# Performance work log

Hardware: AMD Instinct MI355X
Metric: run time of the kernel (lower is better)

## Reference

```python
import math
import jax, jax.numpy as jnp
import numpy as np

CH_IN = 32
CH_OUT = 32
K = 3
P = 4
STRIDE = 2
ITER = 3
FINAL_LAMBDA = 0.01
EPS = 1e-8
LOG_2PI = math.log(2.0 * math.pi)


def _conv_stat(x):
    # Conv2d(ch_in, ch_in, K, stride, bias=False) with constant weight 1/K^2, VALID padding
    w = jnp.full((CH_IN, CH_IN, K, K), 1.0 / (K * K), dtype=x.dtype)
    return jax.lax.conv_general_dilated(
        x, w, window_strides=(STRIDE, STRIDE), padding='VALID',
        dimension_numbers=('NCHW', 'OIHW', 'NCHW'))


def setup_inputs() -> dict:
    key = jax.random.key(0)
    k1, k2, k3 = jax.random.split(key, 3)
    bs, h_in, w_in = 64, 14, 14
    ho = (h_in - K) // STRIDE + 1  # 6
    x = jax.random.normal(k1, (bs, CH_IN, h_in, w_in, P, P), dtype=jnp.float32)
    a = jax.random.uniform(k2, (bs, CH_IN, h_in, w_in), dtype=jnp.float32)
    w = jax.random.uniform(k3, (1, CH_IN, ho, ho, P, P, CH_OUT), dtype=jnp.float32)
    b_u = jnp.zeros((CH_OUT,), jnp.float32)
    b_a = jnp.zeros((CH_OUT,), jnp.float32)
    return {"x": x, "a": a, "w": w, "b_u": b_u, "b_a": b_a}


def _voting(x, w):
    # x: (bs, ci, h_in, w_in, P, P) -> v: (bs, ci, h_out, w_out, P, P, co)
    bs, ci, h, wd = x.shape[:4]
    # raw reshape, matching torch .view on contiguous tensor
    xc = _conv_stat(x.reshape(bs * P * P, ci, h, wd))
    ho, wo = xc.shape[2], xc.shape[3]
    xc = xc.reshape(bs, ci, ho, wo, P, P)
    # repeat x along ch_out, then raw reshape (P,P,co)->(co,P,P), same as torch .view
    xv = jnp.broadcast_to(xc[..., None], (bs, ci, ho, wo, P, P, CH_OUT))
    xv = xv.reshape(bs, ci, ho, wo, CH_OUT, P, P)
    wv = jnp.broadcast_to(w, (bs, ci, ho, wo, P, P, CH_OUT))
    wv = wv.reshape(bs, ci, ho, wo, CH_OUT, P, P)
    v = jnp.matmul(xv, wv)  # batched 4x4 matmuls
    return v.reshape(bs, ci, ho, wo, P, P, CH_OUT)


def _m_step(a, r, v, lambd, b_u, b_a):
    # a: (N, ci, 1)  r: (N, ci, co)  v: (N, ci, co, pp)
    r = (r * a)[..., None] + EPS                                  # (N, ci, co, 1)
    r_sum = jnp.sum(r, axis=1, keepdims=True)                     # (N, 1, co, 1)
    mu = jnp.sum(r * v, axis=1, keepdims=True) / r_sum            # (N, 1, co, pp)
    sig_sq = jnp.sum(r * (v - mu) ** 2, axis=1, keepdims=True) / r_sum + EPS
    cost = (b_u.reshape(1, 1, CH_OUT, 1) + 0.5 * jnp.log(sig_sq)) * r_sum
    a_out = jax.nn.sigmoid(lambd * (b_a.reshape(1, 1, CH_OUT, 1)
                                    - jnp.sum(cost, axis=3, keepdims=True)))
    return a_out, mu, sig_sq


def _e_step(mu, sig_sq, a_out, v):
    p_ln = -(v - mu) ** 2 / (2.0 * sig_sq) - 0.5 * jnp.log(sig_sq) - 0.5 * LOG_2PI
    ap_ln = jnp.sum(p_ln, axis=3, keepdims=True) + jnp.log(a_out)  # (N, ci, co, 1)
    return jax.nn.softmax(ap_ln[..., 0], axis=2)                   # (N, ci, co)


def _em_routing(v, a, b_u, b_a):
    bs, ci, h, wd, p1, p2, co = v.shape
    # raw reshapes, matching torch .view
    vv = v.reshape(bs * h * wd, ci, co, p1 * p2)
    av = a.reshape(bs * h * wd, ci)[..., None]
    r = jnp.full((bs * h * wd, ci, co), 1.0 / co, dtype=v.dtype)
    for it in range(ITER):
        lambd = FINAL_LAMBDA * (1.0 - 0.95 ** (1 + it))
        a_out, mu, sig_sq = _m_step(av, r, vv, lambd, b_u, b_a)
        if it < ITER - 1:
            r = _e_step(mu, sig_sq, a_out, vv)
    mu = mu.reshape(bs, co, h, wd, p1, p2)
    a_out = a_out.reshape(bs, co, h, wd)
    return mu, a_out


def reference(x, a, w, b_u, b_a):
    v = _voting(x, w)
    a_conv = _conv_stat(a)
    mu, a_out = _em_routing(v, a_conv, b_u, b_a)
    return mu, a_out
```

## Files before the change

kernel.cpp:

```cpp
#include <hip/hip_runtime.h>
#include <math.h>


#define EPSF 1e-8f

typedef float f2 __attribute__((ext_vector_type(2)));

__device__ __forceinline__ float rcpf(float x) { return __builtin_amdgcn_rcpf(x); }

__global__ __launch_bounds__(256) void pre_kernel(
        const float* __restrict__ x, const float* __restrict__ a,
        const float* __restrict__ w,
        float* __restrict__ S, float* __restrict__ A, float* __restrict__ Wsum) {
    int bid = blockIdx.x;
    if (bid < 1088) {
        __shared__ float plane[6272];
        __shared__ float bsum[196];
        const int t = threadIdx.x;
        const float* src = (bid < 1024) ? (x + (size_t)bid * 6272)
                                        : (a + (size_t)(bid - 1024) * 6272);
        for (int k = t; k < 1568; k += 256)
            *(float4*)&plane[k * 4] = *(const float4*)(src + k * 4);
        __syncthreads();
        if (t < 196) {
            float s = 0.f;
#pragma unroll
            for (int c = 0; c < 32; ++c) s += plane[c * 196 + t];
            bsum[t] = s;
        }
        __syncthreads();
        if (t < 36) {
            int oy = t / 6, ox = t - oy * 6;
            const float* q = &bsum[oy * 28 + ox * 2];
            float s = (q[0] + q[1] + q[2]) + (q[14] + q[15] + q[16])
                    + (q[28] + q[29] + q[30]);
            s *= (1.0f / 9.0f);
            if (bid < 1024) S[bid * 36 + t] = s;
            else            A[(bid - 1024) * 36 + t] = s;
        }
    } else {
        int wi = (bid - 1088) * 256 + threadIdx.x;
        int sp = wi >> 12;
        int rr = wi & 4095;
        int ci = rr >> 7, co = (rr >> 2) & 31, j = rr & 3;
        int B = sp * 32 + ci;
        int cc = B / 36;
        int rem = B - cc * 36;
        int wbase = cc * 18432 + (rem / 6) * 3072 + (rem % 6) * 512 + co * 16 + j;
        Wsum[wi] = w[wbase] + w[wbase + 4] + w[wbase + 8] + w[wbase + 12];
    }
}

__global__ __launch_bounds__(128, 4) void em_kernel(
        const float* __restrict__ bu, const float* __restrict__ ba,
        const float* __restrict__ S, const float* __restrict__ A,
        const float* __restrict__ Wsum, float* __restrict__ out) {
    __shared__ float Sv[512];
    __shared__ float avs[32];
    __shared__ float lgb[33 * 32];

    const int t = threadIdx.x;
    const int w = t >> 6;
    const int lane = t & 63;
    const int o = w * 16 + (lane & 15);
    const int cq = lane >> 4;
    const int c0 = cq * 8;
    const int n = blockIdx.x;
    const int bq = n / 36;
    const int sp = n - bq * 36;

    if (t < 32) avs[t] = A[bq * 36 + (32 * sp + t) % 36];
    for (int e = t; e < 512; e += 128) {
        int ci = e >> 4, hc2 = e & 15;
        int B = sp * 32 + ci;
        int cc = B / 36;
        int rem = B - cc * 36;
        int off = cc * 576 + (rem / 6) * 96 + (rem % 6) * 16 + hc2;
        int hi = off / 1152;
        int lo = off - hi * 1152;
        Sv[e] = S[(bq * 16 + hi) * 36 + lo % 36];
    }
    __syncthreads();

    const int hc = o >> 1;
    f2 V2[8][2];
    float avr[8], r[8];
    const float* Wn = Wsum + sp * 4096;
#pragma unroll
    for (int cl = 0; cl < 8; ++cl) {
        int c = c0 + cl;
        float sv = Sv[c * 16 + hc];
        float4 w4 = *(const float4*)(Wn + c * 128 + o * 4);
        V2[cl][0] = (f2){sv * w4.x, sv * w4.y};
        V2[cl][1] = (f2){sv * w4.z, sv * w4.w};
        avr[cl] = avs[c];
        r[cl] = 0.03125f;
    }
    const float bu16 = 16.0f * bu[o];
    const float ba_o = ba[o];
    f2 mu2[2], q2[2];
    float aout = 0.f;
    const float lambdas[3] = {5.0e-4f, 9.75e-4f, 1.42625e-3f};

    for (int it = 0; it < 3; ++it) {
        float rp[8];
#pragma unroll
        for (int cl = 0; cl < 8; ++cl) rp[cl] = r[cl] * avr[cl] + EPSF;
        float rs = ((rp[0] + rp[1]) + (rp[2] + rp[3]))
                 + ((rp[4] + rp[5]) + (rp[6] + rp[7]));
        rs += __shfl_xor(rs, 16);
        rs += __shfl_xor(rs, 32);
        float rinv = rcpf(rs);
#pragma unroll
        for (int p = 0; p < 2; ++p) {
            f2 a0 = {0.f, 0.f}, a1 = {0.f, 0.f};
#pragma unroll
            for (int cl = 0; cl < 8; cl += 2) {
                a0 += rp[cl] * V2[cl][p];
                a1 += rp[cl + 1] * V2[cl + 1][p];
            }
            f2 m = a0 + a1;
            m.x += __shfl_xor(m.x, 16); m.x += __shfl_xor(m.x, 32);
            m.y += __shfl_xor(m.y, 16); m.y += __shfl_xor(m.y, 32);
            mu2[p] = m * rinv;
        }
        float L;
        {
            f2 sgv[2];
#pragma unroll
            for (int p = 0; p < 2; ++p) {
                f2 a0 = {0.f, 0.f}, a1 = {0.f, 0.f};
#pragma unroll
                for (int cl = 0; cl < 8; cl += 2) {
                    f2 d0 = V2[cl][p] - mu2[p];
                    f2 d1 = V2[cl + 1][p] - mu2[p];
                    a0 += (d0 * d0) * rp[cl];
                    a1 += (d1 * d1) * rp[cl + 1];
                }
                f2 sg = a0 + a1;
                sg.x += __shfl_xor(sg.x, 16); sg.x += __shfl_xor(sg.x, 32);
                sg.y += __shfl_xor(sg.y, 16); sg.y += __shfl_xor(sg.y, 32);
                sgv[p] = sg * rinv + EPSF;
                q2[p] = (f2){2.0f * rcpf(sgv[p].x), 2.0f * rcpf(sgv[p].y)};
            }
            L = __logf((sgv[0].x * sgv[0].y) * (sgv[1].x * sgv[1].y));
        }
        float cost = (bu16 + 2.0f * L) * rs;
        float z = lambdas[it] * (ba_o - cost);
        aout = rcpf(1.0f + __expf(-z));

        if (it < 2) {
            float T = __logf(aout) - 2.0f * L;
#pragma unroll
            for (int cl = 0; cl < 8; ++cl) {
                f2 d0 = V2[cl][0] - mu2[0];
                f2 d1 = V2[cl][1] - mu2[1];
                f2 s2 = (d0 * d0) * q2[0] + (d1 * d1) * q2[1];
                lgb[(c0 + cl) * 33 + o] = T - (s2.x + s2.y);
            }
            __syncthreads();
            {
                int cT = t >> 2, q = t & 3;
                float* rowp = &lgb[cT * 33 + q * 8];
                float4 u0 = *(float4*)(rowp);
                float4 u1 = *(float4*)(rowp + 4);
                float m0 = fmaxf(fmaxf(u0.x, u0.y), fmaxf(u0.z, u0.w));
                float m1 = fmaxf(fmaxf(u1.x, u1.y), fmaxf(u1.z, u1.w));
                float m = fmaxf(m0, m1);
                m = fmaxf(m, __shfl_xor(m, 1));
                m = fmaxf(m, __shfl_xor(m, 2));
                u0.x = __expf(u0.x - m); u0.y = __expf(u0.y - m);
                u0.z = __expf(u0.z - m); u0.w = __expf(u0.w - m);
                u1.x = __expf(u1.x - m); u1.y = __expf(u1.y - m);
                u1.z = __expf(u1.z - m); u1.w = __expf(u1.w - m);
                float s0 = (u0.x + u0.y) + (u0.z + u0.w);
                float s1 = (u1.x + u1.y) + (u1.z + u1.w);
                float ssum = s0 + s1;
                ssum += __shfl_xor(ssum, 1);
                ssum += __shfl_xor(ssum, 2);
                float inv = rcpf(ssum);
                u0.x *= inv; u0.y *= inv; u0.z *= inv; u0.w *= inv;
                u1.x *= inv; u1.y *= inv; u1.z *= inv; u1.w *= inv;
                *(float4*)(rowp)     = u0;
                *(float4*)(rowp + 4) = u1;
            }
            __syncthreads();
#pragma unroll
            for (int cl = 0; cl < 8; ++cl)
                r[cl] = lgb[(c0 + cl) * 33 + o];
        }
    }

    float4 val = {mu2[0].x, mu2[0].y, mu2[1].x, mu2[1].y};
    float4* po = (float4*)(out + n * 512 + o * 16);
    po[cq] = val;
    if (cq == 0) out[1179648 + n * 32 + o] = aout;
}

extern "C" void kernel_launch(void* const* d_in, const int* in_sizes, int n_in,
                              void* d_out, int out_size, void* d_ws, size_t ws_size,
                              hipStream_t stream) {
    const float* x = (const float*)d_in[0];
    const float* a = (const float*)d_in[1];
    const float* w = (const float*)d_in[2];
    const float* bu = (const float*)d_in[3];
    const float* ba = (const float*)d_in[4];
    float* out = (float*)d_out;

    float* S    = (float*)d_ws;
    float* A    = S + 36864;
    float* Wsum = A + 2304;

    pre_kernel<<<1088 + 576, 256, 0, stream>>>(x, a, w, S, A, Wsum);
    em_kernel<<<2304, 128, 0, stream>>>(bu, ba, S, A, Wsum, out);
}
```

Before: 24.18 us.

## Process two routing positions per em_kernel block to interleave independent work

Each em_kernel block now handles two spatial positions instead of one. Their EM iterations are interleaved so the shuffle reductions, transcendental ops and barriers of the two independent problems can overlap, which raises instruction-level parallelism and halves the block count and barrier count per position. The cost is roughly doubled register and shared-memory use per block (the launch-bounds occupancy hint drops from 4 to 2) and half as many blocks to spread across the GPU.

```diff
diff --git a/kernel.cpp b/kernel.cpp
--- a/kernel.cpp
+++ b/kernel.cpp
@@ -51,13 +51,13 @@
     }
 }
 
-__global__ __launch_bounds__(128, 4) void em_kernel(
+__global__ __launch_bounds__(128, 2) void em_kernel(
         const float* __restrict__ bu, const float* __restrict__ ba,
         const float* __restrict__ S, const float* __restrict__ A,
         const float* __restrict__ Wsum, float* __restrict__ out) {
-    __shared__ float Sv[512];
-    __shared__ float avs[32];
-    __shared__ float lgb[33 * 32];
+    __shared__ float Sv[2][512];
+    __shared__ float avs[2][32];
+    __shared__ float lgb[2][33 * 32];
 
     const int t = threadIdx.x;
     const int w = t >> 6;
@@ -65,136 +65,197 @@
     const int o = w * 16 + (lane & 15);
     const int cq = lane >> 4;
     const int c0 = cq * 8;
-    const int n = blockIdx.x;
-    const int bq = n / 36;
-    const int sp = n - bq * 36;
-
-    if (t < 32) avs[t] = A[bq * 36 + (32 * sp + t) % 36];
-    for (int e = t; e < 512; e += 128) {
-        int ci = e >> 4, hc2 = e & 15;
+    const int n0 = blockIdx.x * 2;
+    const int bq0 = n0 / 36, sp0 = n0 - bq0 * 36;
+    const int n1 = n0 + 1;
+    const int bq1 = n1 / 36, sp1 = n1 - bq1 * 36;
+
+    if (t < 64) {
+        int g = t >> 5, i = t & 31;
+        int bq = g ? bq1 : bq0, sp = g ? sp1 : sp0;
+        avs[g][i] = A[bq * 36 + (32 * sp + i) % 36];
+    }
+    for (int e = t; e < 1024; e += 128) {
+        int g = e >> 9, e2 = e & 511;
+        int bq = g ? bq1 : bq0, sp = g ? sp1 : sp0;
+        int ci = e2 >> 4, hc2 = e2 & 15;
         int B = sp * 32 + ci;
         int cc = B / 36;
         int rem = B - cc * 36;
         int off = cc * 576 + (rem / 6) * 96 + (rem % 6) * 16 + hc2;
         int hi = off / 1152;
         int lo = off - hi * 1152;
-        Sv[e] = S[(bq * 16 + hi) * 36 + lo % 36];
+        Sv[g][e2] = S[(bq * 16 + hi) * 36 + lo % 36];
     }
     __syncthreads();
 
     const int hc = o >> 1;
-    f2 V2[8][2];
-    float avr[8], r[8];
-    const float* Wn = Wsum + sp * 4096;
-#pragma unroll
-    for (int cl = 0; cl < 8; ++cl) {
-        int c = c0 + cl;
-        float sv = Sv[c * 16 + hc];
-        float4 w4 = *(const float4*)(Wn + c * 128 + o * 4);
-        V2[cl][0] = (f2){sv * w4.x, sv * w4.y};
-        V2[cl][1] = (f2){sv * w4.z, sv * w4.w};
-        avr[cl] = avs[c];
-        r[cl] = 0.03125f;
+    f2 V2[2][8][2];
+    float avr[2][8], r[2][8];
+#pragma unroll
+    for (int g = 0; g < 2; ++g) {
+        const float* Wn = Wsum + (g ? sp1 : sp0) * 4096;
+#pragma unroll
+        for (int cl = 0; cl < 8; ++cl) {
+            int c = c0 + cl;
+            float sv = Sv[g][c * 16 + hc];
+            float4 w4 = *(const float4*)(Wn + c * 128 + o * 4);
+            V2[g][cl][0] = (f2){sv * w4.x, sv * w4.y};
+            V2[g][cl][1] = (f2){sv * w4.z, sv * w4.w};
+            avr[g][cl] = avs[g][c];
+            r[g][cl] = 0.03125f;
+        }
     }
     const float bu16 = 16.0f * bu[o];
     const float ba_o = ba[o];
-    f2 mu2[2], q2[2];
-    float aout = 0.f;
+    f2 mu2[2][2], q2[2][2];
+    float aout[2] = {0.f, 0.f};
     const float lambdas[3] = {5.0e-4f, 9.75e-4f, 1.42625e-3f};
 
     for (int it = 0; it < 3; ++it) {
-        float rp[8];
-#pragma unroll
-        for (int cl = 0; cl < 8; ++cl) rp[cl] = r[cl] * avr[cl] + EPSF;
-        float rs = ((rp[0] + rp[1]) + (rp[2] + rp[3]))
-                 + ((rp[4] + rp[5]) + (rp[6] + rp[7]));
-        rs += __shfl_xor(rs, 16);
-        rs += __shfl_xor(rs, 32);
-        float rinv = rcpf(rs);
-#pragma unroll
-        for (int p = 0; p < 2; ++p) {
-            f2 a0 = {0.f, 0.f}, a1 = {0.f, 0.f};
-#pragma unroll
-            for (int cl = 0; cl < 8; cl += 2) {
-                a0 += rp[cl] * V2[cl][p];
-                a1 += rp[cl + 1] * V2[cl + 1][p];
-            }
-            f2 m = a0 + a1;
-            m.x += __shfl_xor(m.x, 16); m.x += __shfl_xor(m.x, 32);
-            m.y += __shfl_xor(m.y, 16); m.y += __shfl_xor(m.y, 32);
-            mu2[p] = m * rinv;
-        }
-        float L;
+        float rp[2][8], rs[2], rinv[2];
+#pragma unroll
+        for (int g = 0; g < 2; ++g) {
+#pragma unroll
+            for (int cl = 0; cl < 8; ++cl) rp[g][cl] = r[g][cl] * avr[g][cl] + EPSF;
+            rs[g] = ((rp[g][0] + rp[g][1]) + (rp[g][2] + rp[g][3]))
+                  + ((rp[g][4] + rp[g][5]) + (rp[g][6] + rp[g][7]));
+        }
+        rs[0] += __shfl_xor(rs[0], 16); rs[1] += __shfl_xor(rs[1], 16);
+        rs[0] += __shfl_xor(rs[0], 32); rs[1] += __shfl_xor(rs[1], 32);
+        rinv[0] = rcpf(rs[0]); rinv[1] = rcpf(rs[1]);
         {
-            f2 sgv[2];
+            f2 m[2][2];
+#pragma unroll
+            for (int g = 0; g < 2; ++g)
 #pragma unroll
             for (int p = 0; p < 2; ++p) {
                 f2 a0 = {0.f, 0.f}, a1 = {0.f, 0.f};
 #pragma unroll
                 for (int cl = 0; cl < 8; cl += 2) {
-                    f2 d0 = V2[cl][p] - mu2[p];
-                    f2 d1 = V2[cl + 1][p] - mu2[p];
-                    a0 += (d0 * d0) * rp[cl];
-                    a1 += (d1 * d1) * rp[cl + 1];
-                }
-                f2 sg = a0 + a1;
-                sg.x += __shfl_xor(sg.x, 16); sg.x += __shfl_xor(sg.x, 32);
-                sg.y += __shfl_xor(sg.y, 16); sg.y += __shfl_xor(sg.y, 32);
-                sgv[p] = sg * rinv + EPSF;
-                q2[p] = (f2){2.0f * rcpf(sgv[p].x), 2.0f * rcpf(sgv[p].y)};
-            }
-            L = __logf((sgv[0].x * sgv[0].y) * (sgv[1].x * sgv[1].y));
-        }
-        float cost = (bu16 + 2.0f * L) * rs;
-        float z = lambdas[it] * (ba_o - cost);
-        aout = rcpf(1.0f + __expf(-z));
+                    a0 += rp[g][cl] * V2[g][cl][p];
+                    a1 += rp[g][cl + 1] * V2[g][cl + 1][p];
+                }
+                m[g][p] = a0 + a1;
+            }
+#pragma unroll
+            for (int g = 0; g < 2; ++g)
+#pragma unroll
+            for (int p = 0; p < 2; ++p) {
+                m[g][p].x += __shfl_xor(m[g][p].x, 16);
+                m[g][p].y += __shfl_xor(m[g][p].y, 16);
+            }
+#pragma unroll
+            for (int g = 0; g < 2; ++g)
+#pragma unroll
+            for (int p = 0; p < 2; ++p) {
+                m[g][p].x += __shfl_xor(m[g][p].x, 32);
+                m[g][p].y += __shfl_xor(m[g][p].y, 32);
+                mu2[g][p] = m[g][p] * rinv[g];
+            }
+        }
+        float L[2];
+        {
+            f2 sg[2][2];
+#pragma unroll
+            for (int g = 0; g < 2; ++g)
+#pragma unroll
+            for (int p = 0; p < 2; ++p) {
+                f2 a0 = {0.f, 0.f}, a1 = {0.f, 0.f};
+#pragma unroll
+                for (int cl = 0; cl < 8; cl += 2) {
+                    f2 d0 = V2[g][cl][p] - mu2[g][p];
+                    f2 d1 = V2[g][cl + 1][p] - mu2[g][p];
+                    a0 += (d0 * d0) * rp[g][cl];
+                    a1 += (d1 * d1) * rp[g][cl + 1];
+                }
+                sg[g][p] = a0 + a1;
+            }
+#pragma unroll
+            for (int g = 0; g < 2; ++g)
+#pragma unroll
+            for (int p = 0; p < 2; ++p) {
+                sg[g][p].x += __shfl_xor(sg[g][p].x, 16);
+                sg[g][p].y += __shfl_xor(sg[g][p].y, 16);
+            }
+#pragma unroll
+            for (int g = 0; g < 2; ++g)
+#pragma unroll
+            for (int p = 0; p < 2; ++p) {
+                sg[g][p].x += __shfl_xor(sg[g][p].x, 32);
+                sg[g][p].y += __shfl_xor(sg[g][p].y, 32);
+                sg[g][p] = sg[g][p] * rinv[g] + EPSF;
+                q2[g][p] = (f2){2.0f * rcpf(sg[g][p].x), 2.0f * rcpf(sg[g][p].y)};
+            }
+#pragma unroll
+            for (int g = 0; g < 2; ++g)
+                L[g] = __logf((sg[g][0].x * sg[g][0].y) * (sg[g][1].x * sg[g][1].y));
+        }
+#pragma unroll
+        for (int g = 0; g < 2; ++g) {
+            float cost = (bu16 + 2.0f * L[g]) * rs[g];
+            float z = lambdas[it] * (ba_o - cost);
+            aout[g] = rcpf(1.0f + __expf(-z));
+        }
 
         if (it < 2) {
-            float T = __logf(aout) - 2.0f * L;
-#pragma unroll
-            for (int cl = 0; cl < 8; ++cl) {
-                f2 d0 = V2[cl][0] - mu2[0];
-                f2 d1 = V2[cl][1] - mu2[1];
-                f2 s2 = (d0 * d0) * q2[0] + (d1 * d1) * q2[1];
-                lgb[(c0 + cl) * 33 + o] = T - (s2.x + s2.y);
+#pragma unroll
+            for (int g = 0; g < 2; ++g) {
+                float T = __logf(aout[g]) - 2.0f * L[g];
+#pragma unroll
+                for (int cl = 0; cl < 8; ++cl) {
+                    f2 d0 = V2[g][cl][0] - mu2[g][0];
+                    f2 d1 = V2[g][cl][1] - mu2[g][1];
+                    f2 s2 = (d0 * d0) * q2[g][0] + (d1 * d1) * q2[g][1];
+                    lgb[g][(c0 + cl) * 33 + o] = T - (s2.x + s2.y);
+                }
             }
             __syncthreads();
             {
                 int cT = t >> 2, q = t & 3;
-                float* rowp = &lgb[cT * 33 + q * 8];
-                float4 u0 = *(float4*)(rowp);
-                float4 u1 = *(float4*)(rowp + 4);
-                float m0 = fmaxf(fmaxf(u0.x, u0.y), fmaxf(u0.z, u0.w));
-                float m1 = fmaxf(fmaxf(u1.x, u1.y), fmaxf(u1.z, u1.w));
-                float m = fmaxf(m0, m1);
-                m = fmaxf(m, __shfl_xor(m, 1));
-                m = fmaxf(m, __shfl_xor(m, 2));
-                u0.x = __expf(u0.x - m); u0.y = __expf(u0.y - m);
-                u0.z = __expf(u0.z - m); u0.w = __expf(u0.w - m);
-                u1.x = __expf(u1.x - m); u1.y = __expf(u1.y - m);
-                u1.z = __expf(u1.z - m); u1.w = __expf(u1.w - m);
-                float s0 = (u0.x + u0.y) + (u0.z + u0.w);
-                float s1 = (u1.x + u1.y) + (u1.z + u1.w);
-                float ssum = s0 + s1;
-                ssum += __shfl_xor(ssum, 1);
-                ssum += __shfl_xor(ssum, 2);
-                float inv = rcpf(ssum);
-                u0.x *= inv; u0.y *= inv; u0.z *= inv; u0.w *= inv;
-                u1.x *= inv; u1.y *= inv; u1.z *= inv; u1.w *= inv;
-                *(float4*)(rowp)     = u0;
-                *(float4*)(rowp + 4) = u1;
+#pragma unroll
+                for (int g = 0; g < 2; ++g) {
+                    float* rowp = &lgb[g][cT * 33 + q * 8];
+                    float4 u0 = *(float4*)(rowp);
+                    float4 u1 = *(float4*)(rowp + 4);
+                    float m0 = fmaxf(fmaxf(u0.x, u0.y), fmaxf(u0.z, u0.w));
+                    float m1 = fmaxf(fmaxf(u1.x, u1.y), fmaxf(u1.z, u1.w));
+                    float m = fmaxf(m0, m1);
+                    m = fmaxf(m, __shfl_xor(m, 1));
+                    m = fmaxf(m, __shfl_xor(m, 2));
+                    u0.x = __expf(u0.x - m); u0.y = __expf(u0.y - m);
+                    u0.z = __expf(u0.z - m); u0.w = __expf(u0.w - m);
+                    u1.x = __expf(u1.x - m); u1.y = __expf(u1.y - m);
+                    u1.z = __expf(u1.z - m); u1.w = __expf(u1.w - m);
+                    float s0 = (u0.x + u0.y) + (u0.z + u0.w);
+                    float s1 = (u1.x + u1.y) + (u1.z + u1.w);
+                    float ssum = s0 + s1;
+                    ssum += __shfl_xor(ssum, 1);
+                    ssum += __shfl_xor(ssum, 2);
+                    float inv = rcpf(ssum);
+                    u0.x *= inv; u0.y *= inv; u0.z *= inv; u0.w *= inv;
+                    u1.x *= inv; u1.y *= inv; u1.z *= inv; u1.w *= inv;
+                    *(float4*)(rowp)     = u0;
+                    *(float4*)(rowp + 4) = u1;
+                }
             }
             __syncthreads();
 #pragma unroll
+            for (int g = 0; g < 2; ++g)
+#pragma unroll
             for (int cl = 0; cl < 8; ++cl)
-                r[cl] = lgb[(c0 + cl) * 33 + o];
-        }
-    }
-
-    float4 val = {mu2[0].x, mu2[0].y, mu2[1].x, mu2[1].y};
-    float4* po = (float4*)(out + n * 512 + o * 16);
-    po[cq] = val;
-    if (cq == 0) out[1179648 + n * 32 + o] = aout;
+                r[g][cl] = lgb[g][(c0 + cl) * 33 + o];
+        }
+    }
+
+#pragma unroll
+    for (int g = 0; g < 2; ++g) {
+        int n = n0 + g;
+        float4 val = {mu2[g][0].x, mu2[g][0].y, mu2[g][1].x, mu2[g][1].y};
+        float4* po = (float4*)(out + n * 512 + o * 16);
+        po[cq] = val;
+        if (cq == 0) out[1179648 + n * 32 + o] = aout[g];
+    }
 }
 
 extern "C" void kernel_launch(void* const* d_in, const int* in_sizes, int n_in,
@@ -212,5 +273,5 @@
     float* Wsum = A + 2304;
 
     pre_kernel<<<1088 + 576, 256, 0, stream>>>(x, a, w, S, A, Wsum);
-    em_kernel<<<2304, 128, 0, stream>>>(bu, ba, S, A, Wsum, out);
+    em_kernel<<<1152, 128, 0, stream>>>(bu, ba, S, A, Wsum, out);
 }
```

Result: slower. 27.07 us (+12.0%).
